# Kernel optimization log

Hardware: AMD Instinct MI355X
Metric: run time of the kernel (lower is better)

Reference implementation:

```python
import jax, jax.numpy as jnp
import numpy as np

D = 1024
H = 16
HD = D // H  # head_dim = 64
B, S = 2, 2048


def setup_inputs() -> dict:
    key = jax.random.key(0)
    ks = jax.random.split(key, 5)
    scale = 1.0 / np.sqrt(D)
    return {
        "sequences": jax.random.normal(ks[0], (B, S, D), dtype=jnp.float32),
        "Wq": jax.random.normal(ks[1], (D, D), dtype=jnp.float32) * scale,
        "bq": jnp.zeros((D,), dtype=jnp.float32),
        "Wk": jax.random.normal(ks[2], (D, D), dtype=jnp.float32) * scale,
        "bk": jnp.zeros((D,), dtype=jnp.float32),
        "Wv": jax.random.normal(ks[3], (D, D), dtype=jnp.float32) * scale,
        "bv": jnp.zeros((D,), dtype=jnp.float32),
        "Wo": jax.random.normal(ks[4], (D, D), dtype=jnp.float32) * scale,
        "bo": jnp.zeros((D,), dtype=jnp.float32),
    }


def _split_heads(x):
    # [B, S, D] -> [B, H, S, HD]
    b, s, _ = x.shape
    return x.reshape(b, s, H, HD).transpose(0, 2, 1, 3)


def reference(sequences, Wq, bq, Wk, bk, Wv, bv, Wo, bo):
    b, s, _ = sequences.shape
    q = _split_heads(sequences @ Wq + bq)  # [B,H,S,HD]
    k = _split_heads(sequences @ Wk + bk)
    v = _split_heads(sequences @ Wv + bv)
    inv_sqrt_hd = jnp.asarray(1.0 / np.sqrt(HD), dtype=sequences.dtype)
    scores = jnp.einsum("bhqd,bhkd->bhqk", q, k) * inv_sqrt_hd  # [B,H,S,S]
    attn = jax.nn.softmax(scores, axis=-1)
    ctx = jnp.einsum("bhqk,bhkd->bhqd", attn, v)  # [B,H,S,HD]
    ctx = ctx.transpose(0, 2, 1, 3).reshape(b, s, D)  # merge heads
    return ctx @ Wo + bo
```

## Files before the change

kernel.cpp:

```cpp
#include <hip/hip_runtime.h>
#include <hip/hip_bf16.h>
#include <cstdint>

#define D 1024
#define H 16
#define HD 64
#define B 2
#define S 2048
#define NTOK (B * S)

typedef __bf16 bf16x8 __attribute__((ext_vector_type(8)));
typedef float f32x4 __attribute__((ext_vector_type(4)));

__device__ __forceinline__ unsigned short f2bf(float x) {
  union { float f; unsigned u; } v; v.f = x;
  unsigned r = v.u + 0x7fffu + ((v.u >> 16) & 1u);
  return (unsigned short)(r >> 16);
}

__device__ __forceinline__ bf16x8 ld16(const unsigned short* p) {
  uint4 u = *reinterpret_cast<const uint4*>(p);
  return __builtin_bit_cast(bf16x8, u);
}

__device__ __forceinline__ void gload_lds16(const unsigned short* g, unsigned short* lds) {
  __builtin_amdgcn_global_load_lds(
      (const __attribute__((address_space(1))) void*)g,
      (__attribute__((address_space(3))) void*)lds, 16, 0, 0);
}

__global__ void k_cvt(const float* __restrict__ x, unsigned short* __restrict__ y, int n4) {
  int i = blockIdx.x * blockDim.x + threadIdx.x;
  if (i >= n4) return;
  float4 v = reinterpret_cast<const float4*>(x)[i];
  ushort4 o;
  o.x = f2bf(v.x); o.y = f2bf(v.y); o.z = f2bf(v.z); o.w = f2bf(v.w);
  reinterpret_cast<ushort4*>(y)[i] = o;
}

__global__ void k_transp(const float* __restrict__ w, unsigned short* __restrict__ wt) {
  __shared__ float t[32][33];
  int tx = threadIdx.x & 31, ty = threadIdx.x >> 5;
  int k0 = blockIdx.x * 32, n0 = blockIdx.y * 32;
#pragma unroll
  for (int i = 0; i < 4; ++i)
    t[ty + 8 * i][tx] = w[(size_t)(k0 + ty + 8 * i) * D + n0 + tx];
  __syncthreads();
#pragma unroll
  for (int i = 0; i < 4; ++i)
    wt[(size_t)(n0 + ty + 8 * i) * D + k0 + tx] = f2bf(t[tx][ty + 8 * i]);
}

__global__ __launch_bounds__(256) void k_gemm_qkv(
    const unsigned short* __restrict__ A,
    const unsigned short* __restrict__ Bt,
    const float* __restrict__ bq, const float* __restrict__ bk, const float* __restrict__ bv,
    unsigned short* __restrict__ Qo, unsigned short* __restrict__ Ko, unsigned short* __restrict__ Vo) {
  constexpr int K = 1024;
  __shared__ __align__(16) unsigned short As[2][128 * 32];
  __shared__ __align__(16) unsigned short Bs[2][128 * 32];
  const int tid = threadIdx.x;
  const int lane = tid & 63;
  const int wave = tid >> 6;
  const int l16 = lane & 15, lg = lane >> 4;
  const int wr = wave >> 1, wc = wave & 1;
  const int m0 = blockIdx.x * 128;
  const int n0 = blockIdx.y * 128;

  const int srow = tid >> 2;
  const int skoff = (tid & 3) * 8;
  const int wbase = wave * 512;

  f32x4 acc[4][4] = {};

  auto stage = [&](int buf, int kt) {
    const unsigned short* ga = A + (size_t)(m0 + srow) * K + kt * 32 + skoff;
    gload_lds16(ga, &As[buf][wbase]);
    gload_lds16(ga + (size_t)64 * K, &As[buf][2048 + wbase]);
    const unsigned short* gb = Bt + (size_t)(n0 + srow) * K + kt * 32 + skoff;
    gload_lds16(gb, &Bs[buf][wbase]);
    gload_lds16(gb + (size_t)64 * K, &Bs[buf][2048 + wbase]);
  };

  stage(0, 0);
  int cur = 0;
  for (int kt = 0; kt < K / 32; ++kt) {
    __syncthreads();
    if (kt + 1 < K / 32) stage(cur ^ 1, kt + 1);
    bf16x8 af[4], bfr[4];
#pragma unroll
    for (int mf = 0; mf < 4; ++mf)
      af[mf] = ld16(&As[cur][(wr * 64 + mf * 16 + l16) * 32 + lg * 8]);
#pragma unroll
    for (int nf = 0; nf < 4; ++nf)
      bfr[nf] = ld16(&Bs[cur][(wc * 64 + nf * 16 + l16) * 32 + lg * 8]);
#pragma unroll
    for (int mf = 0; mf < 4; ++mf)
#pragma unroll
      for (int nf = 0; nf < 4; ++nf)
        acc[mf][nf] = __builtin_amdgcn_mfma_f32_16x16x32_bf16(af[mf], bfr[nf], acc[mf][nf], 0, 0, 0);
    cur ^= 1;
  }

  const int seg = n0 >> 10;
  const float* bp = (seg == 0) ? bq : (seg == 1) ? bk : bv;
  const float osc = 0.18033688011112042f;

#pragma unroll
  for (int mf = 0; mf < 4; ++mf) {
#pragma unroll
    for (int nf = 0; nf < 4; ++nf) {
      const int n = n0 + wc * 64 + nf * 16 + l16;
      const int nl = n & 1023;
      const int h = nl >> 6, hd = nl & 63;
      const int mbase = m0 + wr * 64 + mf * 16 + lg * 4;
      const float bval = bp[nl];
      if (seg == 0) {
#pragma unroll
        for (int r = 0; r < 4; ++r) {
          const int m = mbase + r;
          const int b = m >> 11, s = m & 2047;
          Qo[((size_t)(b * H + h) * S + s) * HD + hd] = f2bf((acc[mf][nf][r] + bval) * osc);
        }
      } else if (seg == 1) {
#pragma unroll
        for (int r = 0; r < 4; ++r) {
          const int m = mbase + r;
          const int b = m >> 11, s = m & 2047;
          const size_t idx = (size_t)(b * H + h) * 131072 + (s >> 6) * 4096 +
                             ((s >> 4) & 3) * 1024 + (hd >> 5) * 512 +
                             ((hd >> 3) & 3) * 128 + (s & 15) * 8 + (hd & 7);
          Ko[idx] = f2bf(acc[mf][nf][r] + bval);
        }
      } else {
        const int b = mbase >> 11, s = mbase & 2047;
        const int d = hd;
        const size_t idx = (size_t)(b * H + h) * 131072 + (s >> 6) * 4096 +
                           (d >> 4) * 1024 + ((s >> 5) & 1) * 512 +
                           ((s >> 3) & 3) * 128 + (d & 15) * 8 + (s & 7);
        ushort4 o;
        o.x = f2bf(acc[mf][nf][0] + bval);
        o.y = f2bf(acc[mf][nf][1] + bval);
        o.z = f2bf(acc[mf][nf][2] + bval);
        o.w = f2bf(acc[mf][nf][3] + bval);
        *reinterpret_cast<ushort4*>(&Vo[idx]) = o;
      }
    }
  }
}

__global__ __launch_bounds__(256) void k_gemm_o(
    const unsigned short* __restrict__ A,
    const unsigned short* __restrict__ Bt,
    const float* __restrict__ bias,
    float* __restrict__ C) {
  constexpr int K = 1024, N = 1024;
  __shared__ __align__(16) unsigned short As[2][64 * 32];
  __shared__ __align__(16) unsigned short Bs[2][128 * 32];
  const int tid = threadIdx.x;
  const int lane = tid & 63;
  const int wave = tid >> 6;
  const int l16 = lane & 15, lg = lane >> 4;
  const int wr = wave >> 1, wc = wave & 1;
  const int m0 = blockIdx.x * 64;
  const int n0 = blockIdx.y * 128;

  const int srow = tid >> 2;
  const int skoff = (tid & 3) * 8;
  const int wbase = wave * 512;

  f32x4 acc[2][4] = {};

  auto stage = [&](int buf, int kt) {
    const unsigned short* ga = A + (size_t)(m0 + srow) * K + kt * 32 + skoff;
    gload_lds16(ga, &As[buf][wbase]);
    const unsigned short* gb = Bt + (size_t)(n0 + srow) * K + kt * 32 + skoff;
    gload_lds16(gb, &Bs[buf][wbase]);
    gload_lds16(gb + (size_t)64 * K, &Bs[buf][2048 + wbase]);
  };

  stage(0, 0);
  int cur = 0;
  for (int kt = 0; kt < K / 32; ++kt) {
    __syncthreads();
    if (kt + 1 < K / 32) stage(cur ^ 1, kt + 1);
    bf16x8 af[2], bfr[4];
#pragma unroll
    for (int mf = 0; mf < 2; ++mf)
      af[mf] = ld16(&As[cur][(wr * 32 + mf * 16 + l16) * 32 + lg * 8]);
#pragma unroll
    for (int nf = 0; nf < 4; ++nf)
      bfr[nf] = ld16(&Bs[cur][(wc * 64 + nf * 16 + l16) * 32 + lg * 8]);
#pragma unroll
    for (int mf = 0; mf < 2; ++mf)
#pragma unroll
      for (int nf = 0; nf < 4; ++nf)
        acc[mf][nf] = __builtin_amdgcn_mfma_f32_16x16x32_bf16(af[mf], bfr[nf], acc[mf][nf], 0, 0, 0);
    cur ^= 1;
  }

#pragma unroll
  for (int mf = 0; mf < 2; ++mf) {
#pragma unroll
    for (int nf = 0; nf < 4; ++nf) {
      const int n = n0 + wc * 64 + nf * 16 + l16;
      const int mbase = m0 + wr * 32 + mf * 16 + lg * 4;
      const float bval = bias[n];
#pragma unroll
      for (int r = 0; r < 4; ++r)
        C[(size_t)(mbase + r) * N + n] = acc[mf][nf][r] + bval;
    }
  }
}

__global__ __launch_bounds__(512, 2) void k_attn(
    const unsigned short* __restrict__ Q,
    const unsigned short* __restrict__ Kimg,
    const unsigned short* __restrict__ Vimg,
    unsigned short* __restrict__ Ctx) {
  const int tid = threadIdx.x;
  const int lane = tid & 63;
  const int wave = tid >> 6;
  const int l16 = lane & 15, lg = lane >> 4;
  const int bh = blockIdx.y;
  const int q0 = blockIdx.x * 256 + wave * 32;

  __shared__ __align__(16) unsigned short KtL[2][4096];
  __shared__ __align__(16) unsigned short VtL[2][4096];
  __shared__ __align__(16) unsigned short Pl[8][2][16][72];

  const unsigned short* Qh = Q + ((size_t)bh * S + q0) * HD;
  const unsigned short* Ksrc = Kimg + (size_t)bh * 131072 + tid * 8;
  const unsigned short* Vsrc = Vimg + (size_t)bh * 131072 + tid * 8;

  bf16x8 qf[2][2];
#pragma unroll
  for (int f = 0; f < 2; ++f)
#pragma unroll
    for (int h = 0; h < 2; ++h)
      qf[f][h] = ld16(Qh + (f * 16 + l16) * HD + h * 32 + lg * 8);

  f32x4 ctx[2][4] = {};
  float m_run[2] = {-1e30f, -1e30f}, l_run[2] = {0.f, 0.f};

  gload_lds16(Ksrc, &KtL[0][tid * 8]);
  gload_lds16(Vsrc, &VtL[0][tid * 8]);
  __syncthreads();

  constexpr int NT = S / 64;
  for (int t = 0; t < NT; ++t) {
    const int cur = t & 1;
    if (t + 1 < NT) {
      gload_lds16(Ksrc + (t + 1) * 4096, &KtL[cur ^ 1][tid * 8]);
      gload_lds16(Vsrc + (t + 1) * 4096, &VtL[cur ^ 1][tid * 8]);
    }

    f32x4 st[2][4];
#pragma unroll
    for (int ks = 0; ks < 4; ++ks) {
      const bf16x8 a0 = ld16(&KtL[cur][ks * 1024 + lane * 8]);
      const bf16x8 a1 = ld16(&KtL[cur][ks * 1024 + 512 + lane * 8]);
#pragma unroll
      for (int f = 0; f < 2; ++f) {
        f32x4 a = {};
        a = __builtin_amdgcn_mfma_f32_16x16x32_bf16(a0, qf[f][0], a, 0, 0, 0);
        a = __builtin_amdgcn_mfma_f32_16x16x32_bf16(a1, qf[f][1], a, 0, 0, 0);
        st[f][ks] = a;
      }
    }

#pragma unroll
    for (int f = 0; f < 2; ++f) {
      float tmax = st[f][0][0];
#pragma unroll
      for (int ks = 0; ks < 4; ++ks)
#pragma unroll
        for (int r = 0; r < 4; ++r)
          tmax = fmaxf(tmax, st[f][ks][r]);
      tmax = fmaxf(tmax, __shfl_xor(tmax, 16));
      tmax = fmaxf(tmax, __shfl_xor(tmax, 32));
      const float m_new = fmaxf(m_run[f], tmax);
      const float scale = exp2f(m_run[f] - m_new);
      l_run[f] *= scale;
#pragma unroll
      for (int dt = 0; dt < 4; ++dt) ctx[f][dt] *= scale;

      float tsum = 0.f;
#pragma unroll
      for (int ks = 0; ks < 4; ++ks) {
        const float p0 = exp2f(st[f][ks][0] - m_new);
        const float p1 = exp2f(st[f][ks][1] - m_new);
        const float p2 = exp2f(st[f][ks][2] - m_new);
        const float p3 = exp2f(st[f][ks][3] - m_new);
        tsum += (p0 + p1) + (p2 + p3);
        ushort4 pk;
        pk.x = f2bf(p0); pk.y = f2bf(p1); pk.z = f2bf(p2); pk.w = f2bf(p3);
        *reinterpret_cast<ushort4*>(&Pl[wave][f][l16][ks * 16 + lg * 4]) = pk;
      }
      tsum += __shfl_xor(tsum, 16);
      tsum += __shfl_xor(tsum, 32);
      l_run[f] += tsum;
      m_run[f] = m_new;
    }

#pragma unroll
    for (int kk = 0; kk < 2; ++kk) {
      const bf16x8 pf0 = ld16(&Pl[wave][0][l16][kk * 32 + lg * 8]);
      const bf16x8 pf1 = ld16(&Pl[wave][1][l16][kk * 32 + lg * 8]);
#pragma unroll
      for (int dt = 0; dt < 4; ++dt) {
        const bf16x8 v = ld16(&VtL[cur][(dt * 2 + kk) * 512 + lane * 8]);
        ctx[0][dt] = __builtin_amdgcn_mfma_f32_16x16x32_bf16(v, pf0, ctx[0][dt], 0, 0, 0);
        ctx[1][dt] = __builtin_amdgcn_mfma_f32_16x16x32_bf16(v, pf1, ctx[1][dt], 0, 0, 0);
      }
    }
    __syncthreads();
  }

  const int b = bh >> 4, h = bh & 15;
#pragma unroll
  for (int f = 0; f < 2; ++f) {
    const float inv_l = 1.0f / l_run[f];
#pragma unroll
    for (int dt = 0; dt < 4; ++dt) {
      ushort4 o;
      o.x = f2bf(ctx[f][dt][0] * inv_l);
      o.y = f2bf(ctx[f][dt][1] * inv_l);
      o.z = f2bf(ctx[f][dt][2] * inv_l);
      o.w = f2bf(ctx[f][dt][3] * inv_l);
      const size_t off =
          ((size_t)(b * S + q0 + f * 16 + l16)) * D + h * HD + dt * 16 + lg * 4;
      *reinterpret_cast<ushort4*>(&Ctx[off]) = o;
    }
  }
}

extern "C" void kernel_launch(void* const* d_in, const int* in_sizes, int n_in,
                              void* d_out, int out_size, void* d_ws, size_t ws_size,
                              hipStream_t stream) {
  const float* x  = (const float*)d_in[0];
  const float* Wq = (const float*)d_in[1];
  const float* bq = (const float*)d_in[2];
  const float* Wk = (const float*)d_in[3];
  const float* bk = (const float*)d_in[4];
  const float* Wv = (const float*)d_in[5];
  const float* bv = (const float*)d_in[6];
  const float* Wo = (const float*)d_in[7];
  const float* bo = (const float*)d_in[8];

  char* ws = (char*)d_ws;
  unsigned short* Xb  = (unsigned short*)(ws);
  unsigned short* Wqt = (unsigned short*)(ws + (8u << 20));
  unsigned short* Wkt = (unsigned short*)(ws + (10u << 20));
  unsigned short* Wvt = (unsigned short*)(ws + (12u << 20));
  unsigned short* Wot = (unsigned short*)(ws + (14u << 20));
  unsigned short* Qb  = (unsigned short*)(ws + (16u << 20));
  unsigned short* Kim = (unsigned short*)(ws + (24u << 20));
  unsigned short* Vim = (unsigned short*)(ws + (32u << 20));
  unsigned short* Cx  = Xb;

  k_cvt<<<4096, 256, 0, stream>>>(x, Xb, NTOK * D / 4);
  dim3 tg(32, 32);
  k_transp<<<tg, 256, 0, stream>>>(Wq, Wqt);
  k_transp<<<tg, 256, 0, stream>>>(Wk, Wkt);
  k_transp<<<tg, 256, 0, stream>>>(Wv, Wvt);
  k_transp<<<tg, 256, 0, stream>>>(Wo, Wot);

  k_gemm_qkv<<<dim3(NTOK / 128, 3 * D / 128), 256, 0, stream>>>(
      Xb, Wqt, bq, bk, bv, Qb, Kim, Vim);

  k_attn<<<dim3(S / 256, B * H), 512, 0, stream>>>(Qb, Kim, Vim, Cx);

  k_gemm_o<<<dim3(NTOK / 64, D / 128), 256, 0, stream>>>(Cx, Wot, bo, (float*)d_out);
}
```

Measured before the change: 248.2 us.

## Halve attention query tile per wave, swizzle blocks, skip redundant rescale

Each wave now handles 16 queries instead of 32, so the attention grid doubles to 512 blocks and launch bounds allow 4 blocks per CU. Block indices are swizzled so that concurrently scheduled blocks share K/V heads. The online-softmax rescale is skipped when no row's max grew, and s_setprio is raised around the PV MFMAs. The bf16 conversion now uses the native cast. Smaller tiles improve occupancy and the fill of the 256 CUs, at the cost of loading each K/V tile twice as often per query.

After: 227.9 us. -8.2%, faster.

```diff
diff --git a/kernel.cpp b/kernel.cpp
--- a/kernel.cpp
+++ b/kernel.cpp
@@ -13,9 +13,8 @@
 typedef float f32x4 __attribute__((ext_vector_type(4)));
 
 __device__ __forceinline__ unsigned short f2bf(float x) {
-  union { float f; unsigned u; } v; v.f = x;
-  unsigned r = v.u + 0x7fffu + ((v.u >> 16) & 1u);
-  return (unsigned short)(r >> 16);
+  __bf16 b = (__bf16)x;
+  return __builtin_bit_cast(unsigned short, b);
 }
 
 __device__ __forceinline__ bf16x8 ld16(const unsigned short* p) {
@@ -213,7 +212,7 @@
   }
 }
 
-__global__ __launch_bounds__(512, 2) void k_attn(
+__global__ __launch_bounds__(512, 4) void k_attn(
     const unsigned short* __restrict__ Q,
     const unsigned short* __restrict__ Kimg,
     const unsigned short* __restrict__ Vimg,
@@ -222,26 +221,25 @@
   const int lane = tid & 63;
   const int wave = tid >> 6;
   const int l16 = lane & 15, lg = lane >> 4;
-  const int bh = blockIdx.y;
-  const int q0 = blockIdx.x * 256 + wave * 32;
+
+  const int lin = blockIdx.y * 16 + blockIdx.x;
+  const int swz = (lin & 7) * 64 + (lin >> 3);
+  const int bh = swz >> 4;
+  const int q0 = (swz & 15) * 128 + wave * 16;
 
   __shared__ __align__(16) unsigned short KtL[2][4096];
   __shared__ __align__(16) unsigned short VtL[2][4096];
-  __shared__ __align__(16) unsigned short Pl[8][2][16][72];
+  __shared__ __align__(16) unsigned short Pl[8][16][72];
 
   const unsigned short* Qh = Q + ((size_t)bh * S + q0) * HD;
   const unsigned short* Ksrc = Kimg + (size_t)bh * 131072 + tid * 8;
   const unsigned short* Vsrc = Vimg + (size_t)bh * 131072 + tid * 8;
 
-  bf16x8 qf[2][2];
-#pragma unroll
-  for (int f = 0; f < 2; ++f)
-#pragma unroll
-    for (int h = 0; h < 2; ++h)
-      qf[f][h] = ld16(Qh + (f * 16 + l16) * HD + h * 32 + lg * 8);
-
-  f32x4 ctx[2][4] = {};
-  float m_run[2] = {-1e30f, -1e30f}, l_run[2] = {0.f, 0.f};
+  const bf16x8 qf0 = ld16(Qh + l16 * HD + lg * 8);
+  const bf16x8 qf1 = ld16(Qh + l16 * HD + 32 + lg * 8);
+
+  f32x4 ctx[4] = {};
+  float m_run = -1e30f, l_run = 0.f;
 
   gload_lds16(Ksrc, &KtL[0][tid * 8]);
   gload_lds16(Vsrc, &VtL[0][tid * 8]);
@@ -255,83 +253,75 @@
       gload_lds16(Vsrc + (t + 1) * 4096, &VtL[cur ^ 1][tid * 8]);
     }
 
-    f32x4 st[2][4];
+    f32x4 st[4];
 #pragma unroll
     for (int ks = 0; ks < 4; ++ks) {
       const bf16x8 a0 = ld16(&KtL[cur][ks * 1024 + lane * 8]);
       const bf16x8 a1 = ld16(&KtL[cur][ks * 1024 + 512 + lane * 8]);
-#pragma unroll
-      for (int f = 0; f < 2; ++f) {
-        f32x4 a = {};
-        a = __builtin_amdgcn_mfma_f32_16x16x32_bf16(a0, qf[f][0], a, 0, 0, 0);
-        a = __builtin_amdgcn_mfma_f32_16x16x32_bf16(a1, qf[f][1], a, 0, 0, 0);
-        st[f][ks] = a;
-      }
-    }
-
-#pragma unroll
-    for (int f = 0; f < 2; ++f) {
-      float tmax = st[f][0][0];
-#pragma unroll
-      for (int ks = 0; ks < 4; ++ks)
-#pragma unroll
-        for (int r = 0; r < 4; ++r)
-          tmax = fmaxf(tmax, st[f][ks][r]);
-      tmax = fmaxf(tmax, __shfl_xor(tmax, 16));
-      tmax = fmaxf(tmax, __shfl_xor(tmax, 32));
-      const float m_new = fmaxf(m_run[f], tmax);
-      const float scale = exp2f(m_run[f] - m_new);
-      l_run[f] *= scale;
-#pragma unroll
-      for (int dt = 0; dt < 4; ++dt) ctx[f][dt] *= scale;
-
-      float tsum = 0.f;
-#pragma unroll
-      for (int ks = 0; ks < 4; ++ks) {
-        const float p0 = exp2f(st[f][ks][0] - m_new);
-        const float p1 = exp2f(st[f][ks][1] - m_new);
-        const float p2 = exp2f(st[f][ks][2] - m_new);
-        const float p3 = exp2f(st[f][ks][3] - m_new);
-        tsum += (p0 + p1) + (p2 + p3);
-        ushort4 pk;
-        pk.x = f2bf(p0); pk.y = f2bf(p1); pk.z = f2bf(p2); pk.w = f2bf(p3);
-        *reinterpret_cast<ushort4*>(&Pl[wave][f][l16][ks * 16 + lg * 4]) = pk;
-      }
-      tsum += __shfl_xor(tsum, 16);
-      tsum += __shfl_xor(tsum, 32);
-      l_run[f] += tsum;
-      m_run[f] = m_new;
-    }
+      f32x4 a = {};
+      a = __builtin_amdgcn_mfma_f32_16x16x32_bf16(a0, qf0, a, 0, 0, 0);
+      a = __builtin_amdgcn_mfma_f32_16x16x32_bf16(a1, qf1, a, 0, 0, 0);
+      st[ks] = a;
+    }
+
+    float tmax = st[0][0];
+#pragma unroll
+    for (int ks = 0; ks < 4; ++ks)
+#pragma unroll
+      for (int r = 0; r < 4; ++r)
+        tmax = fmaxf(tmax, st[ks][r]);
+    tmax = fmaxf(tmax, __shfl_xor(tmax, 16));
+    tmax = fmaxf(tmax, __shfl_xor(tmax, 32));
+    if (__any(tmax > m_run)) {
+      const float m_new = fmaxf(m_run, tmax);
+      const float scale = exp2f(m_run - m_new);
+      l_run *= scale;
+#pragma unroll
+      for (int dt = 0; dt < 4; ++dt) ctx[dt] *= scale;
+      m_run = m_new;
+    }
+
+    float tsum = 0.f;
+#pragma unroll
+    for (int ks = 0; ks < 4; ++ks) {
+      const float p0 = exp2f(st[ks][0] - m_run);
+      const float p1 = exp2f(st[ks][1] - m_run);
+      const float p2 = exp2f(st[ks][2] - m_run);
+      const float p3 = exp2f(st[ks][3] - m_run);
+      tsum += (p0 + p1) + (p2 + p3);
+      ushort4 pk;
+      pk.x = f2bf(p0); pk.y = f2bf(p1); pk.z = f2bf(p2); pk.w = f2bf(p3);
+      *reinterpret_cast<ushort4*>(&Pl[wave][l16][ks * 16 + lg * 4]) = pk;
+    }
+    tsum += __shfl_xor(tsum, 16);
+    tsum += __shfl_xor(tsum, 32);
+    l_run += tsum;
 
 #pragma unroll
     for (int kk = 0; kk < 2; ++kk) {
-      const bf16x8 pf0 = ld16(&Pl[wave][0][l16][kk * 32 + lg * 8]);
-      const bf16x8 pf1 = ld16(&Pl[wave][1][l16][kk * 32 + lg * 8]);
+      const bf16x8 pf = ld16(&Pl[wave][l16][kk * 32 + lg * 8]);
+      __builtin_amdgcn_s_setprio(1);
 #pragma unroll
       for (int dt = 0; dt < 4; ++dt) {
         const bf16x8 v = ld16(&VtL[cur][(dt * 2 + kk) * 512 + lane * 8]);
-        ctx[0][dt] = __builtin_amdgcn_mfma_f32_16x16x32_bf16(v, pf0, ctx[0][dt], 0, 0, 0);
-        ctx[1][dt] = __builtin_amdgcn_mfma_f32_16x16x32_bf16(v, pf1, ctx[1][dt], 0, 0, 0);
+        ctx[dt] = __builtin_amdgcn_mfma_f32_16x16x32_bf16(v, pf, ctx[dt], 0, 0, 0);
       }
+      __builtin_amdgcn_s_setprio(0);
     }
     __syncthreads();
   }
 
   const int b = bh >> 4, h = bh & 15;
-#pragma unroll
-  for (int f = 0; f < 2; ++f) {
-    const float inv_l = 1.0f / l_run[f];
-#pragma unroll
-    for (int dt = 0; dt < 4; ++dt) {
-      ushort4 o;
-      o.x = f2bf(ctx[f][dt][0] * inv_l);
-      o.y = f2bf(ctx[f][dt][1] * inv_l);
-      o.z = f2bf(ctx[f][dt][2] * inv_l);
-      o.w = f2bf(ctx[f][dt][3] * inv_l);
-      const size_t off =
-          ((size_t)(b * S + q0 + f * 16 + l16)) * D + h * HD + dt * 16 + lg * 4;
-      *reinterpret_cast<ushort4*>(&Ctx[off]) = o;
-    }
+  const float inv_l = 1.0f / l_run;
+#pragma unroll
+  for (int dt = 0; dt < 4; ++dt) {
+    ushort4 o;
+    o.x = f2bf(ctx[dt][0] * inv_l);
+    o.y = f2bf(ctx[dt][1] * inv_l);
+    o.z = f2bf(ctx[dt][2] * inv_l);
+    o.w = f2bf(ctx[dt][3] * inv_l);
+    const size_t off = ((size_t)(b * S + q0 + l16)) * D + h * HD + dt * 16 + lg * 4;
+    *reinterpret_cast<ushort4*>(&Ctx[off]) = o;
   }
 }
 
@@ -369,7 +359,7 @@
   k_gemm_qkv<<<dim3(NTOK / 128, 3 * D / 128), 256, 0, stream>>>(
       Xb, Wqt, bq, bk, bv, Qb, Kim, Vim);
 
-  k_attn<<<dim3(S / 256, B * H), 512, 0, stream>>>(Qb, Kim, Vim, Cx);
+  k_attn<<<dim3(S / 128, B * H), 512, 0, stream>>>(Qb, Kim, Vim, Cx);
 
   k_gemm_o<<<dim3(NTOK / 64, D / 128), 256, 0, stream>>>(Cx, Wot, bo, (float*)d_out);
 }
```
